# Kernel optimization log

Hardware: AMD Instinct MI355X
Metric: run time of the kernel (lower is better)

## Reference

```python
import jax, jax.numpy as jnp
import numpy as np

D_MODEL = 192; N_HEAD = 6; N_LEVELS = 3; N_POINTS = 4; D_HEAD = D_MODEL // N_HEAD
W_IMG = 1024.0; H_IMG = 1024.0
STRIDES = (8.0, 16.0, 32.0)
SIGMAS = (4.0, 2.0, 1.0)
N_FREQ = 8


def fourier_pe(coords):
    # coords [..., 2] -> [..., 4*N_FREQ]
    freqs = 2.0 ** jnp.arange(N_FREQ, dtype=jnp.float32)
    x = coords[..., 0:1] * freqs * (2.0 * jnp.pi)
    y = coords[..., 1:2] * freqs * (2.0 * jnp.pi)
    return jnp.concatenate([jnp.sin(x), jnp.cos(x), jnp.sin(y), jnp.cos(y)], axis=-1)


def bilinear_sample(feat, pts):
    # feat [B, H, d_h, Hl, Wl]; pts [B, K, R, H, M, 2] (x, y) in feature-pixel coords
    # zero padding outside the map (torch grid_sample padding_mode='zeros', align_corners=True)
    B, Hh, dh, Hl, Wl = feat.shape
    featf = feat.transpose(0, 1, 3, 4, 2).reshape(B, Hh, Hl * Wl, dh)
    x = pts[..., 0]; y = pts[..., 1]
    x0 = jnp.floor(x); y0 = jnp.floor(y)
    wx1 = x - x0; wy1 = y - y0
    wx0 = 1.0 - wx1; wy0 = 1.0 - wy1
    x0i = x0.astype(jnp.int32); y0i = y0.astype(jnp.int32)
    b_idx = jnp.arange(B)[:, None, None, None, None]
    h_idx = jnp.arange(Hh)[None, None, None, :, None]

    def gather(xi, yi):
        valid = (xi >= 0) & (xi < Wl) & (yi >= 0) & (yi < Hl)
        lin = jnp.clip(yi, 0, Hl - 1) * Wl + jnp.clip(xi, 0, Wl - 1)
        v = featf[b_idx, h_idx, lin]  # [B,K,R,H,M,dh]
        return v * valid[..., None].astype(feat.dtype)

    out = (gather(x0i, y0i) * (wx0 * wy0)[..., None]
           + gather(x0i + 1, y0i) * (wx1 * wy0)[..., None]
           + gather(x0i, y0i + 1) * (wx0 * wy1)[..., None]
           + gather(x0i + 1, y0i + 1) * (wx1 * wy1)[..., None])
    return out


def layernorm(x, g, b, eps=1e-5):
    mu = jnp.mean(x, axis=-1, keepdims=True)
    var = jnp.var(x, axis=-1, keepdims=True)
    return (x - mu) * jax.lax.rsqrt(var + eps) * g + b


def setup_inputs():
    key = jax.random.key(0)
    ks = jax.random.split(key, 16)
    B, K, R = 2, 256, 32
    H4 = W4 = 32
    s = 0.02
    inp = {}
    inp['h'] = jax.random.normal(ks[0], (B, K, D_MODEL), jnp.float32)
    inp['top_indices'] = jax.random.randint(ks[1], (B, K, R), 0, H4 * W4)
    inp['query_coords'] = jax.random.uniform(ks[2], (B, K, 2), jnp.float32) * jnp.array([W_IMG, H_IMG], jnp.float32)
    inp['g'] = jax.random.normal(ks[3], (B, H4 * W4, D_MODEL), jnp.float32)
    inp['L2_proj'] = jax.random.normal(ks[4], (B, D_MODEL, 128, 128), jnp.float32)
    inp['L3_proj'] = jax.random.normal(ks[5], (B, D_MODEL, 64, 64), jnp.float32)
    inp['L4_proj'] = jax.random.normal(ks[6], (B, D_MODEL, 32, 32), jnp.float32)
    inp['w_u_w'] = jax.random.normal(ks[7], (D_MODEL, 2 * D_MODEL + 32), jnp.float32) * s
    inp['w_u_b'] = jnp.zeros((D_MODEL,), jnp.float32)
    inp['ln_u_g'] = jnp.ones((D_MODEL,), jnp.float32)
    inp['ln_u_b'] = jnp.zeros((D_MODEL,), jnp.float32)
    inp['w_delta_w'] = jax.random.normal(ks[8], (N_HEAD * N_LEVELS * N_POINTS * 2, D_MODEL), jnp.float32) * s
    inp['w_delta_b'] = jax.random.normal(ks[9], (N_HEAD * N_LEVELS * N_POINTS * 2,), jnp.float32) * s
    inp['w_a_w'] = jax.random.normal(ks[10], (N_HEAD * N_LEVELS * N_POINTS, D_MODEL), jnp.float32) * s
    inp['w_a_b'] = jnp.zeros((N_HEAD * N_LEVELS * N_POINTS,), jnp.float32)
    inp['w_o_w'] = jax.random.normal(ks[11], (D_MODEL, D_MODEL), jnp.float32) * s
    inp['w_o_b'] = jnp.zeros((D_MODEL,), jnp.float32)
    inp['e_deform'] = jax.random.normal(ks[12], (1, 1, 1, D_MODEL), jnp.float32) * s
    return inp


def reference(h, top_indices, query_coords, g, L2_proj, L3_proj, L4_proj,
              w_u_w, w_u_b, ln_u_g, ln_u_b, w_delta_w, w_delta_b,
              w_a_w, w_a_b, w_o_w, w_o_b, e_deform):
    B, K, d = h.shape
    R = top_indices.shape[2]
    H, d_h, L, M = N_HEAD, D_HEAD, N_LEVELS, N_POINTS
    H4, W4 = L4_proj.shape[2], L4_proj.shape[3]

    # anchor pixel coordinates from L4 indices
    stride_4 = STRIDES[2]
    anchor_x = (top_indices % W4).astype(jnp.float32)
    anchor_y = (top_indices // W4).astype(jnp.float32)
    anchor_px = jnp.stack([anchor_x * stride_4 + stride_4 / 2,
                           anchor_y * stride_4 + stride_4 / 2], axis=-1)  # [B,K,R,2]

    # gather global tokens at anchors
    b_idx = jnp.arange(B)[:, None, None]
    g_r = g[b_idx, top_indices]  # [B,K,R,d]

    # relative position encoding
    delta_p = anchor_px - query_coords[:, :, None, :]
    delta_p_norm = delta_p / jnp.array([W_IMG, H_IMG], jnp.float32)
    phi = fourier_pe(delta_p_norm)  # [B,K,R,32]

    h_exp = jnp.broadcast_to(h[:, :, None, :], (B, K, R, d))
    u_input = jnp.concatenate([h_exp, g_r, phi], axis=-1)  # [B,K,R,2d+32]
    u_r = layernorm(jax.nn.gelu(jnp.einsum('bkrc,dc->bkrd', u_input, w_u_w) + w_u_b,
                                approximate=False), ln_u_g, ln_u_b)

    raw_offsets = (jnp.einsum('bkrd,od->bkro', u_r, w_delta_w) + w_delta_b
                   ).reshape(B, K, R, H, L, M, 2)
    logits = (jnp.einsum('bkrd,od->bkro', u_r, w_a_w) + w_a_b).reshape(B, K, R, H, L * M)
    weights = jax.nn.softmax(logits, axis=-1).reshape(B, K, R, H, L, M)

    proj_maps = [L2_proj, L3_proj, L4_proj]
    h_r = jnp.zeros((B, K, R, H, d_h), h.dtype)
    for l in range(L):
        feat = proj_maps[l]
        Hl, Wl = feat.shape[2], feat.shape[3]
        feat = feat.reshape(B, H, d_h, Hl, Wl)
        anchor_feat = anchor_px / STRIDES[l]  # [B,K,R,2]
        off = jnp.tanh(raw_offsets[:, :, :, :, l]) * SIGMAS[l]  # [B,K,R,H,M,2]
        pts = anchor_feat[:, :, :, None, None, :] + off  # [B,K,R,H,M,2]
        sampled = bilinear_sample(feat, pts)  # [B,K,R,H,M,d_h]
        h_r = h_r + jnp.einsum('bkrhmc,bkrhm->bkrhc', sampled, weights[:, :, :, :, l])

    h_r = h_r.reshape(B, K, R, d)
    deform_tokens = jnp.einsum('bkrd,od->bkro', h_r, w_o_w) + w_o_b + e_deform
    return deform_tokens
```

## Files before the change

kernel.cpp:

```cpp
#include <hip/hip_runtime.h>
#include <hip/hip_bf16.h>

typedef __hip_bfloat16 bf16;
typedef __attribute__((ext_vector_type(8))) short s8b;
typedef __attribute__((ext_vector_type(4))) float f32x4;
typedef __attribute__((ext_vector_type(2))) float v2f;

__device__ __forceinline__ float us2f(unsigned short u) {
  union { unsigned int i; float f; } v; v.i = ((unsigned int)u) << 16; return v.f;
}
__device__ __forceinline__ float ldf(const void* p, int i, bool f32m) {
  return f32m ? ((const float*)p)[i] : us2f(((const unsigned short*)p)[i]);
}
__device__ __forceinline__ bool sniff_f32(const void* ln_g_ones) {
  return ((const unsigned int*)ln_g_ones)[0] == 0x3F800000u;
}
__device__ __forceinline__ short f2bs(float x) {
  bf16 v = __float2bfloat16(x); short s; __builtin_memcpy(&s, &v, 2); return s;
}
__device__ __forceinline__ s8b cvt8(const float* p) {
  s8b r;
  #pragma unroll
  for (int j = 0; j < 8; ++j) r[j] = f2bs(p[j]);
  return r;
}
__device__ __forceinline__ v2f bf2x(unsigned int u) {
  union { unsigned int i; float f; } lo, hi;
  lo.i = u << 16; hi.i = u & 0xffff0000u;
  v2f r; r.x = lo.f; r.y = hi.f; return r;
}

__global__ __launch_bounds__(256) void prep_w(
    const void* __restrict__ wu,  const void* __restrict__ wub,
    const void* __restrict__ lng, const void* __restrict__ lnb,
    const void* __restrict__ wd,  const void* __restrict__ wdb,
    const void* __restrict__ wa,  const void* __restrict__ wab,
    const void* __restrict__ wo,  const void* __restrict__ wob,
    const void* __restrict__ ed,
    bf16* __restrict__ wb1, bf16* __restrict__ wb2, bf16* __restrict__ wb3,
    float* __restrict__ wu_b, float* __restrict__ ln_g, float* __restrict__ ln_b,
    float* __restrict__ wda_b, float* __restrict__ wo_be)
{
  const bool f32m = sniff_f32(lng);
  int i0 = blockIdx.x * 256 + threadIdx.x;
  const int stride = 32 * 256;
  for (int i = i0; i < 192 * 416; i += stride) {
    int d = i / 416, c = i - d * 416;
    int ks = c >> 5, r32 = c & 31, q = r32 >> 3, j = r32 & 7;
    int lane = q * 16 + (d & 15), nt = d >> 4;
    wb1[((ks * 12 + nt) * 64 + lane) * 8 + j] = __float2bfloat16(ldf(wu, i, f32m));
  }
  for (int i = i0; i < 144 * 192; i += stride) {
    int o = i / 192, c = i - o * 192;
    int ks = c >> 5, r32 = c & 31, q = r32 >> 3, j = r32 & 7;
    int lane = q * 16 + (o & 15), nt = o >> 4;
    wb2[((ks * 14 + nt) * 64 + lane) * 8 + j] = __float2bfloat16(ldf(wd, i, f32m));
  }
  for (int i = i0; i < 72 * 192; i += stride) {
    int o = 144 + i / 192, c = i % 192;
    int ks = c >> 5, r32 = c & 31, q = r32 >> 3, j = r32 & 7;
    int lane = q * 16 + (o & 15), nt = o >> 4;
    wb2[((ks * 14 + nt) * 64 + lane) * 8 + j] = __float2bfloat16(ldf(wa, i, f32m));
  }
  for (int i = i0; i < 192 * 192; i += stride) {
    int o = i / 192, dK = i - o * 192;
    int ks = dK >> 5, r32 = dK & 31, q = r32 >> 3, j = r32 & 7;
    int lane = q * 16 + (o & 15), nt = o >> 4;
    wb3[((ks * 12 + nt) * 64 + lane) * 8 + j] = __float2bfloat16(ldf(wo, i, f32m));
  }
  if (i0 < 192) {
    wu_b[i0]  = ldf(wub, i0, f32m);
    ln_g[i0]  = ldf(lng, i0, f32m);
    ln_b[i0]  = ldf(lnb, i0, f32m);
    wo_be[i0] = ldf(wob, i0, f32m) + ldf(ed, i0, f32m);
  }
  if (i0 < 216) wda_b[i0] = (i0 < 144) ? ldf(wdb, i0, f32m) : ldf(wab, i0 - 144, f32m);
}

__global__ __launch_bounds__(256) void prep_feats(
    const void* __restrict__ L2, const void* __restrict__ L3,
    const void* __restrict__ L4, const void* __restrict__ lng,
    bf16* __restrict__ f2, bf16* __restrict__ f3, bf16* __restrict__ f4)
{
  __shared__ float tile[64][65];
  const bool f32m = sniff_f32(lng);
  const int t = threadIdx.x;
  int bid = blockIdx.x;
  const void* src; bf16* dst; int HW, spt;
  if (bid < 1536)      { src = L2; dst = f2; HW = 16384; spt = 256; }
  else if (bid < 1920) { bid -= 1536; src = L3; dst = f3; HW = 4096; spt = 64; }
  else                 { bid -= 1920; src = L4; dst = f4; HW = 1024; spt = 16; }
  int ct = bid % 3; bid /= 3;
  int st = bid % spt; int b = bid / spt;
  int sp0 = st * 64, ch0 = ct * 64;
  int q = t & 3, ch = t >> 2;

  if (f32m) {
    const float* srcf = (const float*)src + (size_t)(b * 192 + ch0 + ch) * HW + sp0;
    #pragma unroll
    for (int i = 0; i < 4; ++i) {
      int p0 = q * 16 + i * 4;
      float4 v = *(const float4*)&srcf[p0];
      tile[p0 + 0][ch] = v.x;
      tile[p0 + 1][ch] = v.y;
      tile[p0 + 2][ch] = v.z;
      tile[p0 + 3][ch] = v.w;
    }
  } else {
    const unsigned short* srcu =
        (const unsigned short*)src + (size_t)(b * 192 + ch0 + ch) * HW + sp0;
    #pragma unroll
    for (int i = 0; i < 4; ++i) {
      int p0 = q * 16 + i * 4;
      #pragma unroll
      for (int k = 0; k < 4; ++k) tile[p0 + k][ch] = us2f(srcu[p0 + k]);
    }
  }
  __syncthreads();
  #pragma unroll
  for (int i = 0; i < 2; ++i) {
    int u = t + 256 * i;
    int p = u >> 3, c8 = u & 7;
    s8b pk = cvt8(&tile[p][c8 * 8]);
    *(s8b*)&dst[(size_t)(b * HW + sp0 + p) * 192 + ch0 + c8 * 8] = pk;
  }
}

__global__ __launch_bounds__(384) void fused_k(
    const int* __restrict__ topi, const void* __restrict__ qc,
    const void* __restrict__ g, const void* __restrict__ h,
    const bf16* __restrict__ wb1, const bf16* __restrict__ wb2,
    const bf16* __restrict__ wb3,
    const float* __restrict__ wu_b,
    const float* __restrict__ ln_g, const float* __restrict__ ln_b,
    const float* __restrict__ wda_b, const float* __restrict__ wo_be,
    const void* __restrict__ lng_raw,
    const bf16* __restrict__ f2, const bf16* __restrict__ f3,
    const bf16* __restrict__ f4,
    const void* __restrict__ L2, const void* __restrict__ L3,
    const void* __restrict__ L4, const int useT,
    float* __restrict__ out)
{
  __shared__ float uni[16 * 216];
  __shared__ float u_sh[16][196];
  __shared__ float anch[16][2];
  __shared__ int   idx_sh[16];
  __shared__ float qxy[2];
  __shared__ float stats[16][2];
  short* gpb = (short*)uni;
  float* ol  = uni;

  const bool f32m = sniff_f32(lng_raw);
  const int t = threadIdx.x;
  const int lane = t & 63, wv = t >> 6;
  const int m16 = lane & 15, quad = lane >> 4;
  const int bk = blockIdx.x >> 1;
  const int b = bk >> 8;
  const int tok0 = blockIdx.x * 16;

  if (t < 2) qxy[t] = ldf(qc, bk * 2 + t, f32m);
  if (t < 16) {
    int idx = topi[tok0 + t];
    idx_sh[t] = idx;
    anch[t][0] = (float)(idx & 31) * 32.f + 16.f;
    anch[t][1] = (float)(idx >> 5) * 32.f + 16.f;
  }
  __syncthreads();

  if (f32m) {
    #pragma unroll
    for (int i = 0; i < 2; ++i) {
      int u = t + 384 * i;
      int r = u / 48, q4 = u - r * 48;
      const float* s4 = (const float*)g + (size_t)(b * 1024 + idx_sh[r]) * 192 + 4 * q4;
      float4 v = *(const float4*)s4;
      short pk[4] = { f2bs(v.x), f2bs(v.y), f2bs(v.z), f2bs(v.w) };
      *(uint2*)&gpb[r * 232 + 4 * q4] = *(const uint2*)pk;
    }
  } else {
    for (int u = t; u < 16 * 192; u += 384) {
      int r = u / 192, j = u - r * 192;
      gpb[r * 232 + j] = f2bs(ldf(g, (b * 1024 + idx_sh[r]) * 192 + j, f32m));
    }
  }
  for (int u = t; u < 16 * 32; u += 384) {
    int r = u >> 5, j = u & 31;
    float dn = (((j & 16) ? (anch[r][1] - qxy[1]) : (anch[r][0] - qxy[0]))) * (1.f / 1024.f);
    float a = dn * (float)(1 << (j & 7)) * 6.283185307179586f;
    gpb[r * 232 + 192 + j] = f2bs((j & 8) ? cosf(a) : sinf(a));
  }
  __syncthreads();

  {
    const s8b* wbv = (const s8b*)wb1;
    const int nt0 = wv * 2, nt1 = wv * 2 + 1;
    float b0 = wu_b[nt0 * 16 + m16], b1 = wu_b[nt1 * 16 + m16];
    f32x4 acc0 = { b0, b0, b0, b0 };
    f32x4 acc1 = { b1, b1, b1, b1 };
    #pragma unroll
    for (int ks = 0; ks < 13; ++ks) {
      s8b a;
      if (ks < 6) {
        if (f32m) {
          const float* hf = (const float*)h + bk * 192 + ks * 32 + quad * 8;
          float4 lo = *(const float4*)hf;
          float4 hi = *(const float4*)(hf + 4);
          float tmp[8] = { lo.x, lo.y, lo.z, lo.w, hi.x, hi.y, hi.z, hi.w };
          a = cvt8(tmp);
        } else {
          a = *(const s8b*)((const unsigned short*)h + bk * 192 + ks * 32 + quad * 8);
        }
      } else {
        a = *(const s8b*)&gpb[m16 * 232 + (ks - 6) * 32 + quad * 8];
      }
      acc0 = __builtin_amdgcn_mfma_f32_16x16x32_bf16(a, wbv[(ks * 12 + nt0) * 64 + lane], acc0, 0, 0, 0);
      acc1 = __builtin_amdgcn_mfma_f32_16x16x32_bf16(a, wbv[(ks * 12 + nt1) * 64 + lane], acc1, 0, 0, 0);
    }
    #pragma unroll
    for (int reg = 0; reg < 4; ++reg) {
      float x0 = acc0[reg], x1 = acc1[reg];
      u_sh[quad * 4 + reg][nt0 * 16 + m16] = 0.5f * x0 * (1.f + erff(x0 * 0.70710678118654752f));
      u_sh[quad * 4 + reg][nt1 * 16 + m16] = 0.5f * x1 * (1.f + erff(x1 * 0.70710678118654752f));
    }
  }
  __syncthreads();

  if (t < 256) {
    int r = t >> 4, i = t & 15;
    float s = 0.f, s2 = 0.f;
    #pragma unroll
    for (int j = 0; j < 12; ++j) { float v = u_sh[r][i * 12 + j]; s += v; s2 += v * v; }
    #pragma unroll
    for (int d = 8; d >= 1; d >>= 1) { s += __shfl_xor(s, d); s2 += __shfl_xor(s2, d); }
    if (i == 0) {
      float mu = s * (1.f / 192.f);
      float var = s2 * (1.f / 192.f) - mu * mu;
      stats[r][0] = mu; stats[r][1] = rsqrtf(var + 1e-5f);
    }
  }
  __syncthreads();
  for (int u = t; u < 16 * 192; u += 384) {
    int r = u / 192, dd = u - r * 192;
    u_sh[r][dd] = (u_sh[r][dd] - stats[r][0]) * stats[r][1] * ln_g[dd] + ln_b[dd];
  }
  __syncthreads();

  {
    s8b afr[6];
    #pragma unroll
    for (int ks = 0; ks < 6; ++ks)
      afr[ks] = cvt8(&u_sh[m16][ks * 32 + quad * 8]);
    const s8b* wbv = (const s8b*)wb2;
    #pragma unroll
    for (int i = 0; i < 3; ++i) {
      int ntile = wv + 6 * i;
      if (ntile < 14) {
        int o0 = ntile * 16 + m16;
        float bias = (o0 < 216) ? wda_b[o0] : 0.f;
        f32x4 acc = { bias, bias, bias, bias };
        #pragma unroll
        for (int ks = 0; ks < 6; ++ks) {
          s8b bfr = wbv[(ks * 14 + ntile) * 64 + lane];
          acc = __builtin_amdgcn_mfma_f32_16x16x32_bf16(afr[ks], bfr, acc, 0, 0, 0);
        }
        if (o0 < 216) {
          #pragma unroll
          for (int reg = 0; reg < 4; ++reg)
            ol[(quad * 4 + reg) * 216 + o0] = acc[reg];
        }
      }
    }
  }
  __syncthreads();

  for (int u = t; u < 16 * 144; u += 384) {
    int r = u / 144, o = u - r * 144;
    int l = (o >> 3) % 3;
    ol[r * 216 + o] = tanhf(ol[r * 216 + o]) * (float)(4 >> l);
  }
  if (t < 96) {
    int r = t / 6, hh = t - r * 6;
    float* lg = &ol[r * 216 + 144 + hh * 12];
    float mx = lg[0];
    for (int i = 1; i < 12; ++i) mx = fmaxf(mx, lg[i]);
    float s = 0.f;
    for (int i = 0; i < 12; ++i) { float e = expf(lg[i] - mx); lg[i] = e; s += e; }
    float inv = 1.f / s;
    for (int i = 0; i < 12; ++i) lg[i] *= inv;
  }
  __syncthreads();

  {
    int tl = t / 24, c8 = t - tl * 24;
    int hc0 = c8 * 8;
    int hh = hc0 >> 5;
    float ax = anch[tl][0], ay = anch[tl][1];
    const float* olp = &ol[tl * 216];
    v2f acc2[4];
    #pragma unroll
    for (int p = 0; p < 4; ++p) { acc2[p].x = 0.f; acc2[p].y = 0.f; }

    const bf16* ftsT[3] = { f2, f3, f4 };
    const void* ftsO[3] = { L2, L3, L4 };
    #pragma unroll
    for (int l = 0; l < 3; ++l) {
      const int Hl = 128 >> l;
      const bf16* ftT = ftsT[l];
      const void* ftO = ftsO[l];
      float inv_s = 1.f / (float)(8 << l);
      float bx = ax * inv_s, by = ay * inv_s;
      #pragma unroll
      for (int m = 0; m < 4; ++m) {
        int ob = ((hh * 3 + l) * 4 + m) * 2;
        float px = bx + olp[ob];
        float py = by + olp[ob + 1];
        float fx = floorf(px), fy = floorf(py);
        int x0 = (int)fx, y0 = (int)fy;
        float wx1 = px - fx, wy1 = py - fy;
        float wx0 = 1.f - wx1, wy0 = 1.f - wy1;
        int xc0 = min(max(x0, 0), Hl - 1),   xc1 = min(max(x0 + 1, 0), Hl - 1);
        int yc0 = min(max(y0, 0), Hl - 1),   yc1 = min(max(y0 + 1, 0), Hl - 1);
        bool vx0 = (x0 >= 0) & (x0 < Hl),    vx1 = (x0 + 1 >= 0) & (x0 + 1 < Hl);
        bool vy0 = (y0 >= 0) & (y0 < Hl),    vy1 = (y0 + 1 >= 0) & (y0 + 1 < Hl);
        float aw = olp[144 + hh * 12 + l * 4 + m];
        float w00 = (vx0 && vy0) ? wx0 * wy0 * aw : 0.f;
        float w01 = (vx1 && vy0) ? wx1 * wy0 * aw : 0.f;
        float w10 = (vx0 && vy1) ? wx0 * wy1 * aw : 0.f;
        float w11 = (vx1 && vy1) ? wx1 * wy1 * aw : 0.f;
        if (useT) {
          uint4 u00 = *(const uint4*)&ftT[((b * Hl + yc0) * Hl + xc0) * 192 + hc0];
          uint4 u01 = *(const uint4*)&ftT[((b * Hl + yc0) * Hl + xc1) * 192 + hc0];
          uint4 u10 = *(const uint4*)&ftT[((b * Hl + yc1) * Hl + xc0) * 192 + hc0];
          uint4 u11 = *(const uint4*)&ftT[((b * Hl + yc1) * Hl + xc1) * 192 + hc0];
          const unsigned int* a0 = (const unsigned int*)&u00;
          const unsigned int* a1 = (const unsigned int*)&u01;
          const unsigned int* a2 = (const unsigned int*)&u10;
          const unsigned int* a3 = (const unsigned int*)&u11;
          #pragma unroll
          for (int p = 0; p < 4; ++p) {
            acc2[p] += bf2x(a0[p]) * w00;
            acc2[p] += bf2x(a1[p]) * w01;
            acc2[p] += bf2x(a2[p]) * w10;
            acc2[p] += bf2x(a3[p]) * w11;
          }
        } else {
          #pragma unroll
          for (int p = 0; p < 4; ++p) {
            #pragma unroll
            for (int e = 0; e < 2; ++e) {
              int ch = hc0 + 2 * p + e;
              float s = ldf(ftO, ((b * 192 + ch) * Hl + yc0) * Hl + xc0, f32m) * w00
                      + ldf(ftO, ((b * 192 + ch) * Hl + yc0) * Hl + xc1, f32m) * w01
                      + ldf(ftO, ((b * 192 + ch) * Hl + yc1) * Hl + xc0, f32m) * w10
                      + ldf(ftO, ((b * 192 + ch) * Hl + yc1) * Hl + xc1, f32m) * w11;
              if (e == 0) acc2[p].x += s; else acc2[p].y += s;
            }
          }
        }
      }
    }
    #pragma unroll
    for (int p = 0; p < 4; ++p) {
      u_sh[tl][hc0 + 2 * p]     = acc2[p].x;
      u_sh[tl][hc0 + 2 * p + 1] = acc2[p].y;
    }
  }
  __syncthreads();

  {
    s8b afr[6];
    #pragma unroll
    for (int ks = 0; ks < 6; ++ks)
      afr[ks] = cvt8(&u_sh[m16][ks * 32 + quad * 8]);
    const s8b* wbv = (const s8b*)wb3;
    #pragma unroll
    for (int nt = 0; nt < 2; ++nt) {
      int ntile = wv * 2 + nt;
      int n = ntile * 16 + m16;
      float bias = wo_be[n];
      f32x4 acc = { bias, bias, bias, bias };
      #pragma unroll
      for (int ks = 0; ks < 6; ++ks) {
        s8b bfr = wbv[(ks * 12 + ntile) * 64 + lane];
        acc = __builtin_amdgcn_mfma_f32_16x16x32_bf16(afr[ks], bfr, acc, 0, 0, 0);
      }
      #pragma unroll
      for (int reg = 0; reg < 4; ++reg)
        out[(long long)(tok0 + quad * 4 + reg) * 192 + n] = acc[reg];
    }
  }
}

extern "C" void kernel_launch(void* const* d_in, const int* in_sizes, int n_in,
                              void* d_out, int out_size, void* d_ws, size_t ws_size,
                              hipStream_t stream)
{
  const void* h    = d_in[0];
  const int*  topi = (const int*)d_in[1];
  const void* qc   = d_in[2];
  const void* g    = d_in[3];
  const void* L2p  = d_in[4];
  const void* L3p  = d_in[5];
  const void* L4p  = d_in[6];
  const void* wu   = d_in[7];
  const void* wub  = d_in[8];
  const void* lng  = d_in[9];
  const void* lnb  = d_in[10];
  const void* wd   = d_in[11];
  const void* wdb  = d_in[12];
  const void* wa   = d_in[13];
  const void* wab  = d_in[14];
  const void* wo   = d_in[15];
  const void* wob  = d_in[16];
  const void* ed   = d_in[17];
  float* outp = (float*)d_out;

  char* ws = (char*)d_ws;
  size_t off = 0;
  auto take = [&](size_t bytes) {
    char* p = ws + off;
    off += (bytes + 255) & ~(size_t)255;
    return p;
  };
  bf16*  wb1     = (bf16*)take(13ULL * 12 * 64 * 8 * 2);
  bf16*  wb2     = (bf16*)take(6ULL * 14 * 64 * 8 * 2);
  bf16*  wb3     = (bf16*)take(6ULL * 12 * 64 * 8 * 2);
  float* wu_bf   = (float*)take(192 * 4);
  float* lngf    = (float*)take(192 * 4);
  float* lnbf    = (float*)take(192 * 4);
  float* wda_b   = (float*)take(216 * 4);
  float* wo_be   = (float*)take(192 * 4);
  size_t feat_bytes = (2ULL * 192 * 128 * 128 + 2ULL * 192 * 64 * 64 + 2ULL * 192 * 32 * 32) * 2 + 1024;
  int useT = (ws_size >= off + feat_bytes) ? 1 : 0;
  bf16* f2 = (bf16*)take(useT ? 2ULL * 192 * 128 * 128 * 2 : 0);
  bf16* f3 = (bf16*)take(useT ? 2ULL * 192 * 64 * 64 * 2 : 0);
  bf16* f4 = (bf16*)take(useT ? 2ULL * 192 * 32 * 32 * 2 : 0);
  (void)in_sizes; (void)n_in; (void)out_size;

  hipLaunchKernelGGL(prep_w, dim3(32), dim3(256), 0, stream,
                     wu, wub, lng, lnb, wd, wdb, wa, wab, wo, wob, ed,
                     wb1, wb2, wb3, wu_bf, lngf, lnbf, wda_b, wo_be);
  if (useT) {
    hipLaunchKernelGGL(prep_feats, dim3(2016), dim3(256), 0, stream,
                       L2p, L3p, L4p, lng, f2, f3, f4);
  }
  hipLaunchKernelGGL(fused_k, dim3(1024), dim3(384), 0, stream,
                     topi, qc, g, h, wb1, wb2, wb3, wu_bf,
                     lngf, lnbf, wda_b, wo_be, lng,
                     f2, f3, f4, L2p, L3p, L4p, useT, outp);
}
```

Baseline: 174.6 us.

## Software-pipeline bilinear gathers and use fast transcendental intrinsics

Restructures the deformable sampling loop on the transposed-feature path so that gathers for the next sampling point are issued before blending the current one, double-buffering the loaded uint4 values to raise memory-level parallelism. Replaces tanhf, expf, division and sinf/cosf with hardware exp, rcp and sin/cos builtins, and adds an occupancy hint to the launch bounds. Also vectorises the shared-memory store of the accumulators. The fast math loses some accuracy, and the occupancy hint may cap registers and cause spills.

```diff
diff --git a/kernel.cpp b/kernel.cpp
--- a/kernel.cpp
+++ b/kernel.cpp
@@ -28,6 +28,16 @@
   union { unsigned int i; float f; } lo, hi;
   lo.i = u << 16; hi.i = u & 0xffff0000u;
   v2f r; r.x = lo.f; r.y = hi.f; return r;
+}
+__device__ __forceinline__ float tanh_fast(float x) {
+  x = fminf(fmaxf(x, -15.f), 15.f);
+  float e = __expf(2.f * x);
+  return (e - 1.f) * __builtin_amdgcn_rcpf(e + 1.f);
+}
+__device__ __forceinline__ void blend8(f32x4& a0, f32x4& a1, uint4 v, float w) {
+  v2f p0 = bf2x(v.x), p1 = bf2x(v.y), p2 = bf2x(v.z), p3 = bf2x(v.w);
+  a0.x += p0.x * w; a0.y += p0.y * w; a0.z += p1.x * w; a0.w += p1.y * w;
+  a1.x += p2.x * w; a1.y += p2.y * w; a1.z += p3.x * w; a1.w += p3.y * w;
 }
 
 __global__ __launch_bounds__(256) void prep_w(
@@ -126,7 +136,7 @@
   }
 }
 
-__global__ __launch_bounds__(384) void fused_k(
+__global__ __launch_bounds__(384, 6) void fused_k(
     const int* __restrict__ topi, const void* __restrict__ qc,
     const void* __restrict__ g, const void* __restrict__ h,
     const bf16* __restrict__ wb1, const bf16* __restrict__ wb2,
@@ -186,8 +196,10 @@
   for (int u = t; u < 16 * 32; u += 384) {
     int r = u >> 5, j = u & 31;
     float dn = (((j & 16) ? (anch[r][1] - qxy[1]) : (anch[r][0] - qxy[0]))) * (1.f / 1024.f);
-    float a = dn * (float)(1 << (j & 7)) * 6.283185307179586f;
-    gpb[r * 232 + 192 + j] = f2bs((j & 8) ? cosf(a) : sinf(a));
+    float rev = dn * (float)(1 << (j & 7));
+    rev = rev - floorf(rev);
+    float v = (j & 8) ? __builtin_amdgcn_cosf(rev) : __builtin_amdgcn_sinf(rev);
+    gpb[r * 232 + 192 + j] = f2bs(v);
   }
   __syncthreads();
 
@@ -276,7 +288,7 @@
   for (int u = t; u < 16 * 144; u += 384) {
     int r = u / 144, o = u - r * 144;
     int l = (o >> 3) % 3;
-    ol[r * 216 + o] = tanhf(ol[r * 216 + o]) * (float)(4 >> l);
+    ol[r * 216 + o] = tanh_fast(ol[r * 216 + o]) * (float)(4 >> l);
   }
   if (t < 96) {
     int r = t / 6, hh = t - r * 6;
@@ -284,8 +296,8 @@
     float mx = lg[0];
     for (int i = 1; i < 12; ++i) mx = fmaxf(mx, lg[i]);
     float s = 0.f;
-    for (int i = 0; i < 12; ++i) { float e = expf(lg[i] - mx); lg[i] = e; s += e; }
-    float inv = 1.f / s;
+    for (int i = 0; i < 12; ++i) { float e = __expf(lg[i] - mx); lg[i] = e; s += e; }
+    float inv = __builtin_amdgcn_rcpf(s);
     for (int i = 0; i < 12; ++i) lg[i] *= inv;
   }
   __syncthreads();
@@ -296,74 +308,110 @@
     int hh = hc0 >> 5;
     float ax = anch[tl][0], ay = anch[tl][1];
     const float* olp = &ol[tl * 216];
-    v2f acc2[4];
-    #pragma unroll
-    for (int p = 0; p < 4; ++p) { acc2[p].x = 0.f; acc2[p].y = 0.f; }
+    f32x4 acc0 = { 0.f, 0.f, 0.f, 0.f };
+    f32x4 acc1 = { 0.f, 0.f, 0.f, 0.f };
 
     const bf16* ftsT[3] = { f2, f3, f4 };
-    const void* ftsO[3] = { L2, L3, L4 };
-    #pragma unroll
-    for (int l = 0; l < 3; ++l) {
-      const int Hl = 128 >> l;
-      const bf16* ftT = ftsT[l];
-      const void* ftO = ftsO[l];
-      float inv_s = 1.f / (float)(8 << l);
-      float bx = ax * inv_s, by = ay * inv_s;
+    if (useT) {
       #pragma unroll
-      for (int m = 0; m < 4; ++m) {
-        int ob = ((hh * 3 + l) * 4 + m) * 2;
-        float px = bx + olp[ob];
-        float py = by + olp[ob + 1];
-        float fx = floorf(px), fy = floorf(py);
-        int x0 = (int)fx, y0 = (int)fy;
-        float wx1 = px - fx, wy1 = py - fy;
-        float wx0 = 1.f - wx1, wy0 = 1.f - wy1;
-        int xc0 = min(max(x0, 0), Hl - 1),   xc1 = min(max(x0 + 1, 0), Hl - 1);
-        int yc0 = min(max(y0, 0), Hl - 1),   yc1 = min(max(y0 + 1, 0), Hl - 1);
-        bool vx0 = (x0 >= 0) & (x0 < Hl),    vx1 = (x0 + 1 >= 0) & (x0 + 1 < Hl);
-        bool vy0 = (y0 >= 0) & (y0 < Hl),    vy1 = (y0 + 1 >= 0) & (y0 + 1 < Hl);
-        float aw = olp[144 + hh * 12 + l * 4 + m];
-        float w00 = (vx0 && vy0) ? wx0 * wy0 * aw : 0.f;
-        float w01 = (vx1 && vy0) ? wx1 * wy0 * aw : 0.f;
-        float w10 = (vx0 && vy1) ? wx0 * wy1 * aw : 0.f;
-        float w11 = (vx1 && vy1) ? wx1 * wy1 * aw : 0.f;
-        if (useT) {
-          uint4 u00 = *(const uint4*)&ftT[((b * Hl + yc0) * Hl + xc0) * 192 + hc0];
-          uint4 u01 = *(const uint4*)&ftT[((b * Hl + yc0) * Hl + xc1) * 192 + hc0];
-          uint4 u10 = *(const uint4*)&ftT[((b * Hl + yc1) * Hl + xc0) * 192 + hc0];
-          uint4 u11 = *(const uint4*)&ftT[((b * Hl + yc1) * Hl + xc1) * 192 + hc0];
-          const unsigned int* a0 = (const unsigned int*)&u00;
-          const unsigned int* a1 = (const unsigned int*)&u01;
-          const unsigned int* a2 = (const unsigned int*)&u10;
-          const unsigned int* a3 = (const unsigned int*)&u11;
+      for (int l = 0; l < 3; ++l) {
+        const int Hl = 128 >> l;
+        const bf16* ftT = ftsT[l];
+        const int bHl = b * Hl;
+        float inv_s = 1.f / (float)(8 << l);
+        float bx = ax * inv_s, by = ay * inv_s;
+
+#define DESC(MM, OFF, WT) do {                                              \
+        int ob = ((hh * 3 + l) * 4 + (MM)) * 2;                             \
+        float px = bx + olp[ob], py = by + olp[ob + 1];                     \
+        float fx = floorf(px), fy = floorf(py);                             \
+        int x0 = (int)fx, y0 = (int)fy;                                     \
+        float wx1 = px - fx, wy1 = py - fy;                                 \
+        float wx0 = 1.f - wx1, wy0 = 1.f - wy1;                             \
+        int xc0 = min(max(x0, 0), Hl - 1), xc1 = min(max(x0 + 1, 0), Hl - 1);\
+        int yc0 = min(max(y0, 0), Hl - 1), yc1 = min(max(y0 + 1, 0), Hl - 1);\
+        bool vx0 = (x0 >= 0) & (x0 < Hl), vx1 = (x0 + 1 >= 0) & (x0 + 1 < Hl);\
+        bool vy0 = (y0 >= 0) & (y0 < Hl), vy1 = (y0 + 1 >= 0) & (y0 + 1 < Hl);\
+        float aw = olp[144 + hh * 12 + l * 4 + (MM)];                       \
+        WT[0] = (vx0 && vy0) ? wx0 * wy0 * aw : 0.f;                        \
+        WT[1] = (vx1 && vy0) ? wx1 * wy0 * aw : 0.f;                        \
+        WT[2] = (vx0 && vy1) ? wx0 * wy1 * aw : 0.f;                        \
+        WT[3] = (vx1 && vy1) ? wx1 * wy1 * aw : 0.f;                        \
+        int r0 = (bHl + yc0) * Hl, r1 = (bHl + yc1) * Hl;                   \
+        OFF[0] = (r0 + xc0) * 192 + hc0;                                    \
+        OFF[1] = (r0 + xc1) * 192 + hc0;                                    \
+        OFF[2] = (r1 + xc0) * 192 + hc0;                                    \
+        OFF[3] = (r1 + xc1) * 192 + hc0;                                    \
+      } while (0)
+
+        int o0_[4], o1_[4], o2_[4], o3_[4];
+        float w0_[4], w1_[4], w2_[4], w3_[4];
+        DESC(0, o0_, w0_);
+        DESC(1, o1_, w1_);
+        uint4 va[4], vb[4];
+        #pragma unroll
+        for (int n = 0; n < 4; ++n) va[n] = *(const uint4*)&ftT[o0_[n]];
+        #pragma unroll
+        for (int n = 0; n < 4; ++n) vb[n] = *(const uint4*)&ftT[o1_[n]];
+        DESC(2, o2_, w2_);
+        DESC(3, o3_, w3_);
+        #pragma unroll
+        for (int n = 0; n < 4; ++n) blend8(acc0, acc1, va[n], w0_[n]);
+        #pragma unroll
+        for (int n = 0; n < 4; ++n) va[n] = *(const uint4*)&ftT[o2_[n]];
+        #pragma unroll
+        for (int n = 0; n < 4; ++n) blend8(acc0, acc1, vb[n], w1_[n]);
+        #pragma unroll
+        for (int n = 0; n < 4; ++n) vb[n] = *(const uint4*)&ftT[o3_[n]];
+        #pragma unroll
+        for (int n = 0; n < 4; ++n) blend8(acc0, acc1, va[n], w2_[n]);
+        #pragma unroll
+        for (int n = 0; n < 4; ++n) blend8(acc0, acc1, vb[n], w3_[n]);
+#undef DESC
+      }
+    } else {
+      const void* ftsO[3] = { L2, L3, L4 };
+      float fa[8] = { 0.f, 0.f, 0.f, 0.f, 0.f, 0.f, 0.f, 0.f };
+      #pragma unroll
+      for (int l = 0; l < 3; ++l) {
+        const int Hl = 128 >> l;
+        const void* ftO = ftsO[l];
+        float inv_s = 1.f / (float)(8 << l);
+        float bx = ax * inv_s, by = ay * inv_s;
+        #pragma unroll
+        for (int m = 0; m < 4; ++m) {
+          int ob = ((hh * 3 + l) * 4 + m) * 2;
+          float px = bx + olp[ob];
+          float py = by + olp[ob + 1];
+          float fx = floorf(px), fy = floorf(py);
+          int x0 = (int)fx, y0 = (int)fy;
+          float wx1 = px - fx, wy1 = py - fy;
+          float wx0 = 1.f - wx1, wy0 = 1.f - wy1;
+          int xc0 = min(max(x0, 0), Hl - 1),   xc1 = min(max(x0 + 1, 0), Hl - 1);
+          int yc0 = min(max(y0, 0), Hl - 1),   yc1 = min(max(y0 + 1, 0), Hl - 1);
+          bool vx0 = (x0 >= 0) & (x0 < Hl),    vx1 = (x0 + 1 >= 0) & (x0 + 1 < Hl);
+          bool vy0 = (y0 >= 0) & (y0 < Hl),    vy1 = (y0 + 1 >= 0) & (y0 + 1 < Hl);
+          float aw = olp[144 + hh * 12 + l * 4 + m];
+          float w00 = (vx0 && vy0) ? wx0 * wy0 * aw : 0.f;
+          float w01 = (vx1 && vy0) ? wx1 * wy0 * aw : 0.f;
+          float w10 = (vx0 && vy1) ? wx0 * wy1 * aw : 0.f;
+          float w11 = (vx1 && vy1) ? wx1 * wy1 * aw : 0.f;
           #pragma unroll
-          for (int p = 0; p < 4; ++p) {
-            acc2[p] += bf2x(a0[p]) * w00;
-            acc2[p] += bf2x(a1[p]) * w01;
-            acc2[p] += bf2x(a2[p]) * w10;
-            acc2[p] += bf2x(a3[p]) * w11;
-          }
-        } else {
-          #pragma unroll
-          for (int p = 0; p < 4; ++p) {
-            #pragma unroll
-            for (int e = 0; e < 2; ++e) {
-              int ch = hc0 + 2 * p + e;
-              float s = ldf(ftO, ((b * 192 + ch) * Hl + yc0) * Hl + xc0, f32m) * w00
-                      + ldf(ftO, ((b * 192 + ch) * Hl + yc0) * Hl + xc1, f32m) * w01
-                      + ldf(ftO, ((b * 192 + ch) * Hl + yc1) * Hl + xc0, f32m) * w10
-                      + ldf(ftO, ((b * 192 + ch) * Hl + yc1) * Hl + xc1, f32m) * w11;
-              if (e == 0) acc2[p].x += s; else acc2[p].y += s;
-            }
+          for (int e = 0; e < 8; ++e) {
+            int ch = hc0 + e;
+            float s = ldf(ftO, ((b * 192 + ch) * Hl + yc0) * Hl + xc0, f32m) * w00
+                    + ldf(ftO, ((b * 192 + ch) * Hl + yc0) * Hl + xc1, f32m) * w01
+                    + ldf(ftO, ((b * 192 + ch) * Hl + yc1) * Hl + xc0, f32m) * w10
+                    + ldf(ftO, ((b * 192 + ch) * Hl + yc1) * Hl + xc1, f32m) * w11;
+            fa[e] += s;
           }
         }
       }
-    }
-    #pragma unroll
-    for (int p = 0; p < 4; ++p) {
-      u_sh[tl][hc0 + 2 * p]     = acc2[p].x;
-      u_sh[tl][hc0 + 2 * p + 1] = acc2[p].y;
-    }
+      acc0.x = fa[0]; acc0.y = fa[1]; acc0.z = fa[2]; acc0.w = fa[3];
+      acc1.x = fa[4]; acc1.y = fa[5]; acc1.z = fa[6]; acc1.w = fa[7];
+    }
+    *(f32x4*)&u_sh[tl][hc0]     = acc0;
+    *(f32x4*)&u_sh[tl][hc0 + 4] = acc1;
   }
   __syncthreads();
 
```

Measured after the change: 274.8 us. 57.4% more time.
